# Performance work log

Measured on AMD Instinct MI355X. Metric: run time of the kernel, lower is better.

Reference implementation:

```python
import jax, jax.numpy as jnp
import numpy as np

NUM_SAMPLES = 100  # hard-coded in the original forward


def _bilinear(img, x, y):
    """Bilinear sample img (H,W) at pixel coords x,y (any shape); border padding.
    Matches F.grid_sample(align_corners=True, padding_mode='border') since the
    original normalizes by (W-1)/(H-1) which maps back to the same pixel coords."""
    H, W = img.shape
    x0 = jnp.floor(x); y0 = jnp.floor(y)
    wx = x - x0; wy = y - y0
    x0i = jnp.clip(x0, 0, W - 1).astype(jnp.int32)
    x1i = jnp.clip(x0 + 1, 0, W - 1).astype(jnp.int32)
    y0i = jnp.clip(y0, 0, H - 1).astype(jnp.int32)
    y1i = jnp.clip(y0 + 1, 0, H - 1).astype(jnp.int32)
    return (img[y0i, x0i] * (1 - wx) * (1 - wy)
            + img[y0i, x1i] * wx * (1 - wy)
            + img[y1i, x0i] * (1 - wx) * wy
            + img[y1i, x1i] * wx * wy)


def setup_inputs() -> dict:
    key = jax.random.key(0)
    k1, k2, k3 = jax.random.split(key, 3)
    H = W = 2048
    N = 100000
    distance_image = jax.random.uniform(k1, (H, W), dtype=jnp.float32)
    points = jax.random.uniform(k2, (N, 2), dtype=jnp.float32) * (H - 1)
    normals = jax.random.normal(k3, (N, 2), dtype=jnp.float32)
    return {"distance_image": distance_image, "points": points, "normals": normals}


def reference(distance_image, points, normals):
    H, W = distance_image.shape
    N = points.shape[0]
    # original clamps both coords to [0, max(H-1, W-1)]
    pts = jnp.clip(points, 0.0, float(max(H - 1, W - 1)))  # (N,2)

    # direction perpendicular to normal, normalized
    d = jnp.stack([-normals[:, 1], normals[:, 0]], axis=-1)
    d = d / jnp.linalg.norm(d, axis=-1, keepdims=True)  # (N,2)
    dx, dy = d[:, 0], d[:, 1]
    px, py = pts[:, 0], pts[:, 1]

    maxf = jnp.finfo(d.dtype).max
    sdx = jnp.where(dx != 0, dx, 1.0)
    sdy = jnp.where(dy != 0, dy, 1.0)
    t_left = jnp.where(dx != 0, (0.0 - px) / sdx, -maxf)
    t_right = jnp.where(dx != 0, (W - 1.0 - px) / sdx, maxf)
    t_top = jnp.where(dy != 0, (0.0 - py) / sdy, -maxf)
    t_bottom = jnp.where(dy != 0, (H - 1.0 - py) / sdy, maxf)
    t_min = jnp.maximum(t_left, t_top)
    t_max = jnp.minimum(t_right, t_bottom)

    p1 = pts + t_min[:, None] * d  # (N,2)
    p2 = pts + t_max[:, None] * d  # (N,2)

    ts = jnp.linspace(0.0, 1.0, NUM_SAMPLES, dtype=pts.dtype)  # (S,)
    line = p1[:, None, :] + ts[None, :, None] * (p2 - p1)[:, None, :]  # (N,S,2)
    lx = jnp.clip(line[..., 0], 0.0, W - 1.0)
    ly = jnp.clip(line[..., 1], 0.0, H - 1.0)
    line = jnp.stack([lx, ly], axis=-1)  # clamped sampled points (N,S,2)

    vals = _bilinear(distance_image, lx, ly)  # (N,S)
    ref_val = _bilinear(distance_image, px, py)  # (N,)

    # local minima: strict minimum vs both neighbors, indices shifted by +1
    center = vals[:, 1:-1]
    minima = (center < vals[:, :-2]) & (center < vals[:, 2:])  # (N,S-2)

    # distance from each candidate (interior sample points) to the reference point
    dist = jnp.linalg.norm(line[:, 1:-1, :] - pts[:, None, :], axis=-1)  # (N,S-2)
    dist = jnp.where(minima, dist, jnp.inf)
    nearest = jnp.argmin(dist, axis=1)  # (N,)
    nearest_val = vals[jnp.arange(N), nearest + 1]  # (N,)

    # per-point mse of two scalars, then mean over points
    return jnp.mean((nearest_val - ref_val) ** 2)
```

## Files before the change

kernel.cpp:

```cpp
#include <hip/hip_runtime.h>
#include <float.h>
#include <math.h>

#define NSAMP 100
#define IMG_W 2048
#define IMG_H 2048

typedef _Float16 h2_t __attribute__((ext_vector_type(2), aligned(4)));
typedef _Float16 h4_t __attribute__((ext_vector_type(4), aligned(8)));
typedef _Float16 h8_t __attribute__((ext_vector_type(8), aligned(16)));

__global__ __launch_bounds__(256) void convert_kernel(const float* __restrict__ in,
                                                      h2_t* __restrict__ V,
                                                      double* __restrict__ accum,
                                                      unsigned int* __restrict__ done) {
    int idx = blockIdx.x * blockDim.x + threadIdx.x;
    if (idx == 0) { *accum = 0.0; *done = 0u; }
    int y  = idx >> 9;
    int x4 = (idx & 511) << 2;
    int y1 = min(y + 1, IMG_H - 1);
    float4 a = *(const float4*)(in + (size_t)y  * IMG_W + x4);
    float4 b = *(const float4*)(in + (size_t)y1 * IMG_W + x4);
    h8_t o;
    o[0] = (_Float16)a.x; o[1] = (_Float16)b.x;
    o[2] = (_Float16)a.y; o[3] = (_Float16)b.y;
    o[4] = (_Float16)a.z; o[5] = (_Float16)b.z;
    o[6] = (_Float16)a.w; o[7] = (_Float16)b.w;
    *(h8_t*)(V + (size_t)y * IMG_W + x4) = o;
}

__device__ __forceinline__ float bilinV(const h2_t* __restrict__ V, float x, float y) {
    float x0f = floorf(x), y0f = floorf(y);
    float wx = x - x0f, wy = y - y0f;
    int x0 = (int)x0f;
    int y0 = (int)y0f;
    int xa = min(x0, IMG_W - 2);
    bool edge = (x0 == IMG_W - 1);
    h4_t q = *(const h4_t*)(V + (size_t)y0 * IMG_W + xa);
    float v00 = edge ? (float)q[2] : (float)q[0];
    float v10 = edge ? (float)q[3] : (float)q[1];
    float v01 = (float)q[2];
    float v11 = (float)q[3];
    return v00 * (1.f - wx) * (1.f - wy) + v01 * wx * (1.f - wy)
         + v10 * (1.f - wx) * wy       + v11 * wx * wy;
}

__device__ __forceinline__ float tparam(int s) {
    return (s == NSAMP - 1) ? 1.0f : (float)((double)s * (1.0 / 99.0));
}

__global__ __launch_bounds__(256) void contour_loss_kernel(
        const h2_t* __restrict__ V,
        const float* __restrict__ points,
        const float* __restrict__ normals,
        double* __restrict__ accum,
        unsigned int* __restrict__ done,
        float* __restrict__ out,
        int N, int nblocks) {
    int i = blockIdx.x * blockDim.x + threadIdx.x;
    float sq = 0.f;
    if (i < N) {
        float px = fminf(fmaxf(points[2 * i],     0.f), 2047.f);
        float py = fminf(fmaxf(points[2 * i + 1], 0.f), 2047.f);
        float nx = normals[2 * i];
        float ny = normals[2 * i + 1];
        float ddx = -ny, ddy = nx;
        float nrm = sqrtf(ddx * ddx + ddy * ddy);
        float dx = ddx / nrm, dy = ddy / nrm;

        const float maxf = FLT_MAX;
        float sdx = (dx != 0.f) ? dx : 1.f;
        float sdy = (dy != 0.f) ? dy : 1.f;
        float t_left   = (dx != 0.f) ? (0.f    - px) / sdx : -maxf;
        float t_right  = (dx != 0.f) ? (2047.f - px) / sdx :  maxf;
        float t_top    = (dy != 0.f) ? (0.f    - py) / sdy : -maxf;
        float t_bottom = (dy != 0.f) ? (2047.f - py) / sdy :  maxf;
        float t_min = fmaxf(t_left, t_top);
        float t_max = fminf(t_right, t_bottom);

        float p1x = px + t_min * dx, p1y = py + t_min * dy;
        float p2x = px + t_max * dx, p2y = py + t_max * dy;
        float vx = p2x - p1x, vy = p2y - p1y;

        float ref_val = bilinV(V, px, py);

        float lx = fminf(fmaxf(p1x, 0.f), 2047.f);
        float ly = fminf(fmaxf(p1y, 0.f), 2047.f);
        float v_im1 = bilinV(V, lx, ly);
        float t1 = tparam(1);
        lx = fminf(fmaxf(p1x + t1 * vx, 0.f), 2047.f);
        ly = fminf(fmaxf(p1y + t1 * vy, 0.f), 2047.f);
        float v_i = bilinV(V, lx, ly);
        float cx = lx, cy = ly;

        float best_val = v_i;
        float best_d2  = INFINITY;

        #pragma unroll 8
        for (int s = 2; s < NSAMP; ++s) {
            float ts = tparam(s);
            float nlx = fminf(fmaxf(p1x + ts * vx, 0.f), 2047.f);
            float nly = fminf(fmaxf(p1y + ts * vy, 0.f), 2047.f);
            float v_ip1 = bilinV(V, nlx, nly);
            if (v_i < v_im1 && v_i < v_ip1) {
                float ex = cx - px, ey = cy - py;
                float d2 = ex * ex + ey * ey;
                if (d2 < best_d2) { best_d2 = d2; best_val = v_i; }
            }
            v_im1 = v_i; v_i = v_ip1; cx = nlx; cy = nly;
        }
        float diff = best_val - ref_val;
        sq = diff * diff;
    }

    for (int off = 32; off > 0; off >>= 1)
        sq += __shfl_down(sq, off);
    __shared__ float wsum[4];
    int lane = threadIdx.x & 63;
    int wid  = threadIdx.x >> 6;
    if (lane == 0) wsum[wid] = sq;
    __syncthreads();
    if (threadIdx.x == 0) {
        float bs = wsum[0] + wsum[1] + wsum[2] + wsum[3];
        atomicAdd(accum, (double)bs);
        __threadfence();
        unsigned int prev = atomicAdd(done, 1u);
        if (prev == (unsigned int)(nblocks - 1)) {
            double total = atomicAdd(accum, 0.0);
            out[0] = (float)(total / (double)N);
        }
    }
}

extern "C" void kernel_launch(void* const* d_in, const int* in_sizes, int n_in,
                              void* d_out, int out_size, void* d_ws, size_t ws_size,
                              hipStream_t stream) {
    const float* img     = (const float*)d_in[0];
    const float* points  = (const float*)d_in[1];
    const float* normals = (const float*)d_in[2];
    int N = in_sizes[1] / 2;
    float* out = (float*)d_out;

    char* ws = (char*)d_ws;
    h2_t* V = (h2_t*)ws;
    size_t off = (size_t)IMG_W * IMG_H * sizeof(h2_t);
    double* accum      = (double*)(ws + off);  off += 8;
    unsigned int* done = (unsigned int*)(ws + off);

    int conv_blocks = (IMG_W * IMG_H / 4) / 256;
    convert_kernel<<<conv_blocks, 256, 0, stream>>>(img, V, accum, done);

    int grid = (N + 255) / 256;
    contour_loss_kernel<<<grid, 256, 0, stream>>>(V, points, normals,
                                                  accum, done, out, N, grid);
}
```

Measured before the change: 128.8 us.

## Split sample lines into segments binned by image region per XCD

Each point's 100-sample line is split into four segments. Each segment is binned by the image region (one of 8) around its midpoint, and worker blocks pull segments from the region queue matched to their XCC ID, so each chiplet's L2 sees a localized part of the fp16 image. Partial per-segment minima are written out and merged in a separate reduce kernel that applies the argmin tie-break by sample index. This adds four kernel launches, atomics-based queues, and extra global traffic for records, in exchange for better cache locality and more parallelism.

```diff
diff --git a/kernel.cpp b/kernel.cpp
--- a/kernel.cpp
+++ b/kernel.cpp
@@ -5,6 +5,9 @@
 #define NSAMP 100
 #define IMG_W 2048
 #define IMG_H 2048
+#define SEG 25
+#define NSEG 4
+#define NREG 8
 
 typedef _Float16 h2_t __attribute__((ext_vector_type(2), aligned(4)));
 typedef _Float16 h4_t __attribute__((ext_vector_type(4), aligned(8)));
@@ -13,9 +16,12 @@
 __global__ __launch_bounds__(256) void convert_kernel(const float* __restrict__ in,
                                                       h2_t* __restrict__ V,
                                                       double* __restrict__ accum,
-                                                      unsigned int* __restrict__ done) {
+                                                      unsigned int* __restrict__ done,
+                                                      unsigned int* __restrict__ qhead,
+                                                      unsigned int* __restrict__ qcnt) {
     int idx = blockIdx.x * blockDim.x + threadIdx.x;
     if (idx == 0) { *accum = 0.0; *done = 0u; }
+    if (idx < NREG) { qhead[idx] = 0u; qcnt[idx] = 0u; }
     int y  = idx >> 9;
     int x4 = (idx & 511) << 2;
     int y1 = min(y + 1, IMG_H - 1);
@@ -27,6 +33,109 @@
     o[4] = (_Float16)a.z; o[5] = (_Float16)b.z;
     o[6] = (_Float16)a.w; o[7] = (_Float16)b.w;
     *(h8_t*)(V + (size_t)y * IMG_W + x4) = o;
+}
+
+__device__ __forceinline__ float tparam(int s) {
+    return (s == NSAMP - 1) ? 1.0f : (float)((double)s * (1.0 / 99.0));
+}
+
+__device__ __forceinline__ void chord(float px, float py, float nx, float ny,
+                                      float& p1x, float& p1y, float& vx, float& vy) {
+    float ddx = -ny, ddy = nx;
+    float nrm = sqrtf(ddx * ddx + ddy * ddy);
+    float dx = ddx / nrm, dy = ddy / nrm;
+    const float maxf = FLT_MAX;
+    float sdx = (dx != 0.f) ? dx : 1.f;
+    float sdy = (dy != 0.f) ? dy : 1.f;
+    float t_left   = (dx != 0.f) ? (0.f    - px) / sdx : -maxf;
+    float t_right  = (dx != 0.f) ? (2047.f - px) / sdx :  maxf;
+    float t_top    = (dy != 0.f) ? (0.f    - py) / sdy : -maxf;
+    float t_bottom = (dy != 0.f) ? (2047.f - py) / sdy :  maxf;
+    float t_min = fmaxf(t_left, t_top);
+    float t_max = fminf(t_right, t_bottom);
+    p1x = px + t_min * dx; p1y = py + t_min * dy;
+    float p2x = px + t_max * dx, p2y = py + t_max * dy;
+    vx = p2x - p1x; vy = p2y - p1y;
+}
+
+__global__ __launch_bounds__(256) void bin_kernel(const float* __restrict__ points,
+                                                  const float* __restrict__ normals,
+                                                  float4* __restrict__ pts4,
+                                                  unsigned int* __restrict__ regs,
+                                                  unsigned int* __restrict__ qcnt,
+                                                  int N) {
+    __shared__ unsigned int lh[NREG];
+    if (threadIdx.x < NREG) lh[threadIdx.x] = 0u;
+    __syncthreads();
+    int i = blockIdx.x * blockDim.x + threadIdx.x;
+    if (i < N) {
+        float px = fminf(fmaxf(points[2 * i],     0.f), 2047.f);
+        float py = fminf(fmaxf(points[2 * i + 1], 0.f), 2047.f);
+        float nx = normals[2 * i];
+        float ny = normals[2 * i + 1];
+        pts4[i] = make_float4(px, py, nx, ny);
+        float p1x, p1y, vx, vy;
+        chord(px, py, nx, ny, p1x, p1y, vx, vy);
+        unsigned int packed = 0;
+        #pragma unroll
+        for (int seg = 0; seg < NSEG; ++seg) {
+            int s_begin = SEG * seg;
+            int s_end   = min(s_begin + SEG + 1, NSAMP - 1);
+            float f = (float)(s_begin + s_end) * 0.5f / 99.0f;
+            float mx = fminf(fmaxf(p1x + f * vx, 0.f), 2047.f);
+            float my = fminf(fmaxf(p1y + f * vy, 0.f), 2047.f);
+            unsigned int r = ((unsigned int)my >> 10) * 4u + ((unsigned int)mx >> 9);
+            packed |= r << (8 * seg);
+            atomicAdd(&lh[r], 1u);
+        }
+        regs[i] = packed;
+    }
+    __syncthreads();
+    if (threadIdx.x < NREG && lh[threadIdx.x]) atomicAdd(&qcnt[threadIdx.x], lh[threadIdx.x]);
+}
+
+__global__ void scan_kernel(const unsigned int* __restrict__ qcnt,
+                            unsigned int* __restrict__ segoff,
+                            unsigned int* __restrict__ cursor) {
+    if (threadIdx.x == 0) {
+        unsigned int run = 0;
+        for (int r = 0; r < NREG; ++r) {
+            segoff[r] = run;
+            cursor[r] = run;
+            run += qcnt[r];
+        }
+    }
+}
+
+__global__ __launch_bounds__(256) void scatter_kernel(const unsigned int* __restrict__ regs,
+                                                      unsigned int* __restrict__ cursor,
+                                                      unsigned int* __restrict__ seglist,
+                                                      int N) {
+    __shared__ unsigned int lh[NREG];
+    __shared__ unsigned int lbase[NREG];
+    if (threadIdx.x < NREG) lh[threadIdx.x] = 0u;
+    __syncthreads();
+    int i = blockIdx.x * blockDim.x + threadIdx.x;
+    unsigned int packed = 0, rank[NSEG];
+    if (i < N) {
+        packed = regs[i];
+        #pragma unroll
+        for (int seg = 0; seg < NSEG; ++seg) {
+            unsigned int r = (packed >> (8 * seg)) & 0xFFu;
+            rank[seg] = atomicAdd(&lh[r], 1u);
+        }
+    }
+    __syncthreads();
+    if (threadIdx.x < NREG)
+        lbase[threadIdx.x] = lh[threadIdx.x] ? atomicAdd(&cursor[threadIdx.x], lh[threadIdx.x]) : 0u;
+    __syncthreads();
+    if (i < N) {
+        #pragma unroll
+        for (int seg = 0; seg < NSEG; ++seg) {
+            unsigned int r = (packed >> (8 * seg)) & 0xFFu;
+            seglist[lbase[r] + rank[seg]] = (unsigned int)(i * 4 + seg);
+        }
+    }
 }
 
 __device__ __forceinline__ float bilinV(const h2_t* __restrict__ V, float x, float y) {
@@ -45,74 +154,100 @@
          + v10 * (1.f - wx) * wy       + v11 * wx * wy;
 }
 
-__device__ __forceinline__ float tparam(int s) {
-    return (s == NSAMP - 1) ? 1.0f : (float)((double)s * (1.0 / 99.0));
-}
-
-__global__ __launch_bounds__(256) void contour_loss_kernel(
+__global__ __launch_bounds__(256) void contour_seg_kernel(
         const h2_t* __restrict__ V,
-        const float* __restrict__ points,
-        const float* __restrict__ normals,
-        double* __restrict__ accum,
-        unsigned int* __restrict__ done,
-        float* __restrict__ out,
-        int N, int nblocks) {
+        const float4* __restrict__ pts4,
+        const unsigned int* __restrict__ seglist,
+        const unsigned int* __restrict__ segoff,
+        const unsigned int* __restrict__ qcnt,
+        unsigned int* __restrict__ qhead,
+        float4* __restrict__ rec) {
+    __shared__ unsigned int s_chunk;
+    unsigned int xcc;
+    asm volatile("s_getreg_b32 %0, hwreg(HW_REG_XCC_ID)" : "=s"(xcc));
+    xcc &= 7u;
+
+    for (int pass = 0; pass < NREG; ++pass) {
+        unsigned int q = (xcc + (unsigned int)pass) & 7u;
+        unsigned int qn = qcnt[q];
+        unsigned int qo = segoff[q];
+        while (true) {
+            if (threadIdx.x == 0) s_chunk = atomicAdd(&qhead[q], 256u);
+            __syncthreads();
+            unsigned int c = s_chunk;
+            __syncthreads();
+            if (c >= qn) break;
+            unsigned int j = c + threadIdx.x;
+            if (j < qn) {
+                unsigned int e = seglist[qo + j];
+                int i  = (int)(e >> 2);
+                int seg = (int)(e & 3u);
+                float4 pt = pts4[i];
+                float px = pt.x, py = pt.y;
+                float p1x, p1y, vx, vy;
+                chord(px, py, pt.z, pt.w, p1x, p1y, vx, vy);
+
+                float ref_val = 0.f;
+                if (seg == 0) ref_val = bilinV(V, px, py);
+
+                int s_begin = SEG * seg;
+                int s_end   = min(s_begin + SEG + 1, NSAMP - 1);
+
+                float tt = tparam(s_begin);
+                float lx = fminf(fmaxf(p1x + tt * vx, 0.f), 2047.f);
+                float ly = fminf(fmaxf(p1y + tt * vy, 0.f), 2047.f);
+                float v_im1 = bilinV(V, lx, ly);
+                tt = tparam(s_begin + 1);
+                lx = fminf(fmaxf(p1x + tt * vx, 0.f), 2047.f);
+                ly = fminf(fmaxf(p1y + tt * vy, 0.f), 2047.f);
+                float v_i = bilinV(V, lx, ly);
+                float cx = lx, cy = ly;
+
+                float best_d2  = INFINITY;
+                float best_idx = 1.0e9f;
+                float best_val = 0.f;
+                if (seg == 0) {
+                    best_idx = 0.f;
+                    best_val = v_i;
+                }
+
+                #pragma unroll 5
+                for (int s = s_begin + 2; s <= s_end; ++s) {
+                    float ts = tparam(s);
+                    float nlx = fminf(fmaxf(p1x + ts * vx, 0.f), 2047.f);
+                    float nly = fminf(fmaxf(p1y + ts * vy, 0.f), 2047.f);
+                    float v_ip1 = bilinV(V, nlx, nly);
+                    if (v_i < v_im1 && v_i < v_ip1) {
+                        float ex = cx - px, ey = cy - py;
+                        float d2 = ex * ex + ey * ey;
+                        if (d2 < best_d2) { best_d2 = d2; best_idx = (float)(s - 1); best_val = v_i; }
+                    }
+                    v_im1 = v_i; v_i = v_ip1; cx = nlx; cy = nly;
+                }
+                rec[e] = make_float4(best_d2, best_idx, best_val, ref_val);
+            }
+        }
+    }
+}
+
+__global__ __launch_bounds__(256) void reduce_kernel(const float4* __restrict__ rec,
+                                                     double* __restrict__ accum,
+                                                     unsigned int* __restrict__ done,
+                                                     float* __restrict__ out,
+                                                     int N, int nblocks) {
     int i = blockIdx.x * blockDim.x + threadIdx.x;
     float sq = 0.f;
     if (i < N) {
-        float px = fminf(fmaxf(points[2 * i],     0.f), 2047.f);
-        float py = fminf(fmaxf(points[2 * i + 1], 0.f), 2047.f);
-        float nx = normals[2 * i];
-        float ny = normals[2 * i + 1];
-        float ddx = -ny, ddy = nx;
-        float nrm = sqrtf(ddx * ddx + ddy * ddy);
-        float dx = ddx / nrm, dy = ddy / nrm;
-
-        const float maxf = FLT_MAX;
-        float sdx = (dx != 0.f) ? dx : 1.f;
-        float sdy = (dy != 0.f) ? dy : 1.f;
-        float t_left   = (dx != 0.f) ? (0.f    - px) / sdx : -maxf;
-        float t_right  = (dx != 0.f) ? (2047.f - px) / sdx :  maxf;
-        float t_top    = (dy != 0.f) ? (0.f    - py) / sdy : -maxf;
-        float t_bottom = (dy != 0.f) ? (2047.f - py) / sdy :  maxf;
-        float t_min = fmaxf(t_left, t_top);
-        float t_max = fminf(t_right, t_bottom);
-
-        float p1x = px + t_min * dx, p1y = py + t_min * dy;
-        float p2x = px + t_max * dx, p2y = py + t_max * dy;
-        float vx = p2x - p1x, vy = p2y - p1y;
-
-        float ref_val = bilinV(V, px, py);
-
-        float lx = fminf(fmaxf(p1x, 0.f), 2047.f);
-        float ly = fminf(fmaxf(p1y, 0.f), 2047.f);
-        float v_im1 = bilinV(V, lx, ly);
-        float t1 = tparam(1);
-        lx = fminf(fmaxf(p1x + t1 * vx, 0.f), 2047.f);
-        ly = fminf(fmaxf(p1y + t1 * vy, 0.f), 2047.f);
-        float v_i = bilinV(V, lx, ly);
-        float cx = lx, cy = ly;
-
-        float best_val = v_i;
-        float best_d2  = INFINITY;
-
-        #pragma unroll 8
-        for (int s = 2; s < NSAMP; ++s) {
-            float ts = tparam(s);
-            float nlx = fminf(fmaxf(p1x + ts * vx, 0.f), 2047.f);
-            float nly = fminf(fmaxf(p1y + ts * vy, 0.f), 2047.f);
-            float v_ip1 = bilinV(V, nlx, nly);
-            if (v_i < v_im1 && v_i < v_ip1) {
-                float ex = cx - px, ey = cy - py;
-                float d2 = ex * ex + ey * ey;
-                if (d2 < best_d2) { best_d2 = d2; best_val = v_i; }
-            }
-            v_im1 = v_i; v_i = v_ip1; cx = nlx; cy = nly;
-        }
-        float diff = best_val - ref_val;
+        float4 best = rec[4 * i];
+        float ref = best.w;
+        #pragma unroll
+        for (int k = 1; k < NSEG; ++k) {
+            float4 r = rec[4 * i + k];
+            if (r.x < best.x || (r.x == best.x && r.y < best.y)) best = r;
+        }
+        float diff = best.z - ref;
         sq = diff * diff;
     }
-
     for (int off = 32; off > 0; off >>= 1)
         sq += __shfl_down(sq, off);
     __shared__ float wsum[4];
@@ -144,13 +279,29 @@
     char* ws = (char*)d_ws;
     h2_t* V = (h2_t*)ws;
     size_t off = (size_t)IMG_W * IMG_H * sizeof(h2_t);
-    double* accum      = (double*)(ws + off);  off += 8;
-    unsigned int* done = (unsigned int*)(ws + off);
+    double* accum        = (double*)(ws + off);       off += 8;
+    unsigned int* done   = (unsigned int*)(ws + off); off += 8;
+    unsigned int* qhead  = (unsigned int*)(ws + off); off += NREG * 4;
+    unsigned int* qcnt   = (unsigned int*)(ws + off); off += NREG * 4;
+    unsigned int* segoff = (unsigned int*)(ws + off); off += NREG * 4;
+    unsigned int* cursor = (unsigned int*)(ws + off); off += NREG * 4;
+    off = (off + 15) & ~(size_t)15;
+    float4* pts4         = (float4*)(ws + off);       off += (size_t)N * 16;
+    unsigned int* regs   = (unsigned int*)(ws + off); off += (size_t)N * 4;
+    unsigned int* seglist= (unsigned int*)(ws + off); off += (size_t)N * NSEG * 4;
+    off = (off + 15) & ~(size_t)15;
+    float4* rec          = (float4*)(ws + off);
 
     int conv_blocks = (IMG_W * IMG_H / 4) / 256;
-    convert_kernel<<<conv_blocks, 256, 0, stream>>>(img, V, accum, done);
-
-    int grid = (N + 255) / 256;
-    contour_loss_kernel<<<grid, 256, 0, stream>>>(V, points, normals,
-                                                  accum, done, out, N, grid);
-}
+    convert_kernel<<<conv_blocks, 256, 0, stream>>>(img, V, accum, done, qhead, qcnt);
+
+    int pgrid = (N + 255) / 256;
+    bin_kernel<<<pgrid, 256, 0, stream>>>(points, normals, pts4, regs, qcnt, N);
+    scan_kernel<<<1, 64, 0, stream>>>(qcnt, segoff, cursor);
+    scatter_kernel<<<pgrid, 256, 0, stream>>>(regs, cursor, seglist, N);
+
+    contour_seg_kernel<<<2048, 256, 0, stream>>>(V, pts4, seglist, segoff, qcnt, qhead, rec);
+
+    int rgrid = (N + 255) / 256;
+    reduce_kernel<<<rgrid, 256, 0, stream>>>(rec, accum, done, out, N, rgrid);
+}
```

Result: slower. 318.1 us (+146.9%).

## Split per-point sample scan into four interleaved chains for more loads in flight

Applied to the files above, without the earlier changes.

Splits the 100-sample scan along each line into four independent segments that advance together, each keeping its own local-minimum state. The segments are merged at the end, with ties broken by sample index to keep argmin semantics. The aim is more independent gather loads in flight per thread, to hide memory latency on the random image reads. The cost is higher register pressure, a few redundant boundary samples, and extra merge logic.

```diff
diff --git a/kernel.cpp b/kernel.cpp
--- a/kernel.cpp
+++ b/kernel.cpp
@@ -1,6 +1,7 @@
 #include <hip/hip_runtime.h>
 #include <float.h>
 #include <math.h>
+#include <limits.h>
 
 #define NSAMP 100
 #define IMG_W 2048
@@ -84,31 +85,68 @@
 
         float ref_val = bilinV(V, px, py);
 
-        float lx = fminf(fmaxf(p1x, 0.f), 2047.f);
-        float ly = fminf(fmaxf(p1y, 0.f), 2047.f);
-        float v_im1 = bilinV(V, lx, ly);
-        float t1 = tparam(1);
-        lx = fminf(fmaxf(p1x + t1 * vx, 0.f), 2047.f);
-        ly = fminf(fmaxf(p1y + t1 * vy, 0.f), 2047.f);
-        float v_i = bilinV(V, lx, ly);
-        float cx = lx, cy = ly;
+        const int sb[4] = {0, 25, 50, 75};
+        const int se[4] = {26, 51, 76, 99};
 
-        float best_val = v_i;
-        float best_d2  = INFINITY;
+        float vm1[4], vi[4], cxx[4], cyy[4];
+        float bd2[4], bval[4];
+        int   bidx[4];
 
-        #pragma unroll 8
-        for (int s = 2; s < NSAMP; ++s) {
-            float ts = tparam(s);
-            float nlx = fminf(fmaxf(p1x + ts * vx, 0.f), 2047.f);
-            float nly = fminf(fmaxf(p1y + ts * vy, 0.f), 2047.f);
-            float v_ip1 = bilinV(V, nlx, nly);
-            if (v_i < v_im1 && v_i < v_ip1) {
-                float ex = cx - px, ey = cy - py;
-                float d2 = ex * ex + ey * ey;
-                if (d2 < best_d2) { best_d2 = d2; best_val = v_i; }
+        #pragma unroll
+        for (int st = 0; st < 4; ++st) {
+            float tt = tparam(sb[st]);
+            float lx = fminf(fmaxf(p1x + tt * vx, 0.f), 2047.f);
+            float ly = fminf(fmaxf(p1y + tt * vy, 0.f), 2047.f);
+            vm1[st] = bilinV(V, lx, ly);
+            tt = tparam(sb[st] + 1);
+            lx = fminf(fmaxf(p1x + tt * vx, 0.f), 2047.f);
+            ly = fminf(fmaxf(p1y + tt * vy, 0.f), 2047.f);
+            vi[st] = bilinV(V, lx, ly);
+            cxx[st] = lx; cyy[st] = ly;
+            bd2[st] = INFINITY;
+            bidx[st] = INT_MAX;
+            bval[st] = 0.f;
+        }
+        bidx[0] = 0;
+        bval[0] = vi[0];
+
+        #pragma unroll 5
+        for (int k = 0; k < 25; ++k) {
+            float vn[4];
+            float nlx[4], nly[4];
+            #pragma unroll
+            for (int st = 0; st < 4; ++st) {
+                if (st < 3 || k < 23) {
+                    int s = sb[st] + 2 + k;
+                    float ts = tparam(s);
+                    nlx[st] = fminf(fmaxf(p1x + ts * vx, 0.f), 2047.f);
+                    nly[st] = fminf(fmaxf(p1y + ts * vy, 0.f), 2047.f);
+                    vn[st] = bilinV(V, nlx[st], nly[st]);
+                }
             }
-            v_im1 = v_i; v_i = v_ip1; cx = nlx; cy = nly;
+            #pragma unroll
+            for (int st = 0; st < 4; ++st) {
+                if (st < 3 || k < 23) {
+                    int s = sb[st] + 2 + k;
+                    if (vi[st] < vm1[st] && vi[st] < vn[st]) {
+                        float ex = cxx[st] - px, ey = cyy[st] - py;
+                        float d2 = ex * ex + ey * ey;
+                        if (d2 < bd2[st]) { bd2[st] = d2; bidx[st] = s - 1; bval[st] = vi[st]; }
+                    }
+                    vm1[st] = vi[st]; vi[st] = vn[st];
+                    cxx[st] = nlx[st]; cyy[st] = nly[st];
+                }
+            }
         }
+
+        float best_d2 = bd2[0]; int best_idx = bidx[0]; float best_val = bval[0];
+        #pragma unroll
+        for (int st = 1; st < 4; ++st) {
+            if (bd2[st] < best_d2 || (bd2[st] == best_d2 && bidx[st] < best_idx)) {
+                best_d2 = bd2[st]; best_idx = bidx[st]; best_val = bval[st];
+            }
+        }
+
         float diff = best_val - ref_val;
         sq = diff * diff;
     }
```

Result: slower. 141.5 us (+9.9%).
